# Optimization experiments

Measured on AMD Instinct MI355X. Metric: run time of the kernel, lower is better.

Reference implementation:

```python
import jax, jax.numpy as jnp
import numpy as np

WH, WW = 7, 7
N = WH * WW
DIM = 128
NH = 4
HD = DIM // NH
B_IMG, NW = 64, 64
B_ = B_IMG * NW

def _relative_position_index():
    ch = np.arange(WH)
    cw = np.arange(WW)
    coords = np.stack(np.meshgrid(ch, cw, indexing='ij'))  # (2, Wh, Ww)
    coords = coords.reshape(2, -1)  # (2, N)
    rel = coords[:, :, None] - coords[:, None, :]  # (2, N, N)
    rel = rel.transpose(1, 2, 0)  # (N, N, 2)
    rel[:, :, 0] += WH - 1
    rel[:, :, 1] += WW - 1
    rel[:, :, 0] *= 2 * WW - 1
    return jnp.asarray(rel.sum(-1), dtype=jnp.int32)  # (N, N)

REL_IDX = _relative_position_index()

def setup_inputs() -> dict:
    key = jax.random.key(0)
    k1, k2, k3, k4, k5 = jax.random.split(key, 5)
    return {
        'x': jax.random.normal(k1, (B_, N, DIM), dtype=jnp.float32),
        'mask': jax.random.normal(k2, (NW, N, N), dtype=jnp.float32),
        'qkv_w': jax.random.normal(k3, (3 * DIM, DIM), dtype=jnp.float32) * 0.02,
        'qkv_b': jax.random.normal(k4, (3 * DIM,), dtype=jnp.float32) * 0.02,
        'rel_table': jax.random.normal(k5, ((2 * WH - 1) * (2 * WW - 1), NH), dtype=jnp.float32) * 0.02,
    }

def reference(x, mask, qkv_w, qkv_b, rel_table):
    B_tot, n, c = x.shape
    scale = HD ** (-0.5)
    # qkv projection; torch split order is (nH, hD, qkv) innermost-to-outermost
    qkv = x @ qkv_w.T + qkv_b                      # (B_, N, 3C)
    qkv = qkv.reshape(B_tot, n, NH, HD, 3)
    q = jnp.transpose(qkv[..., 0], (0, 2, 1, 3))   # (B_, nH, N, hD)
    k = jnp.transpose(qkv[..., 1], (0, 2, 1, 3))
    v = jnp.transpose(qkv[..., 2], (0, 2, 1, 3))
    attn = jnp.einsum('bhnd,bhmd->bhnm', q, k) * scale  # (B_, nH, N, N)
    bias = jnp.transpose(rel_table[REL_IDX.reshape(-1)].reshape(n, n, NH), (2, 0, 1))
    attn = attn + bias[None]
    nW = mask.shape[0]
    attn = attn.reshape(B_tot // nW, nW, NH, n, n) + mask[None, :, None]
    attn = attn.reshape(B_tot, NH, n, n)
    attn = jax.nn.softmax(attn, axis=-1)
    out = jnp.einsum('bhnm,bhmd->bhnd', attn, v)   # (B_, nH, N, hD)
    return jnp.transpose(out, (0, 2, 1, 3)).reshape(B_tot, n, c)
```

## Files before the change

### kernel.cpp

```cpp
#include <hip/hip_runtime.h>


typedef short bf16x8 __attribute__((ext_vector_type(8)));
typedef float f32x4 __attribute__((ext_vector_type(4)));

#define DEVI __device__ __forceinline__

DEVI unsigned short f2b(float f) {
    unsigned u = __builtin_bit_cast(unsigned, f);
    u += 0x7fffu + ((u >> 16) & 1u);
    return (unsigned short)(u >> 16);
}

DEVI unsigned pack2(float lo, float hi) {
    return (unsigned)f2b(lo) | ((unsigned)f2b(hi) << 16);
}

#define WS_BIAS_OFF 98304
#define WS_COMB_OFF 131072
#define COMB_ELEMS  802816u
#define WS_NEED     (131072u + COMB_ELEMS * 4u)

__global__ __launch_bounds__(256) void prep_kernel(
    const float* __restrict__ qkvw, const float* __restrict__ qkvb,
    const float* __restrict__ maskg, const float* __restrict__ relt,
    unsigned short* __restrict__ wb, float* __restrict__ bb,
    float* __restrict__ comb)
{
    const int g = blockIdx.x * 256 + threadIdx.x;
    if (g < 49152) {
        const int row = g >> 7, col = g & 127;
        const int s = row >> 7, r7 = row & 127, hh = r7 >> 5, d = r7 & 31;
        const int c = hh * 96 + d * 3 + s;
        const float mul = (s == 0) ? 0.17677669529663687f : 1.0f;
        wb[row * 128 + col] = f2b(qkvw[c * 128 + col] * mul);
    } else if (g < 49536) {
        const int row = g - 49152;
        const int s = row >> 7, r7 = row & 127, hh = r7 >> 5, d = r7 & 31;
        const int c = hh * 96 + d * 3 + s;
        const float mul = (s == 0) ? 0.17677669529663687f : 1.0f;
        bb[row] = qkvb[c] * mul;
    } else {
        const unsigned g2 = (unsigned)(g - 49536);
        if (g2 < COMB_ELEMS) {
            const int wh = g2 / 3136;
            const int rr = g2 - wh * 3136;
            const int m = rr >> 6, n = rr & 63;
            const int w = wh >> 2, hh = wh & 3;
            float v = -1e30f;
            if (n < 49) {
                const int md = m / 7, mm = m - md * 7;
                const int nd = n / 7, nm = n - nd * 7;
                const int ridx = (md - nd + 6) * 13 + (mm - nm + 6);
                v = maskg[w * 2401 + m * 49 + n] + relt[ridx * 4 + hh];
            }
            comb[g2] = v;
        }
    }
}

struct __align__(16) SmemWS {
    unsigned short kk[4][64][32];
    union {
        unsigned short xs[64][136];
        unsigned short vt[4][32][72];
    } b;
};

__global__ __launch_bounds__(512, 6) void wattn_ws(
    const float* __restrict__ xg, const unsigned short* __restrict__ wb,
    const float* __restrict__ bb, const float* __restrict__ comb,
    float* __restrict__ outg)
{
    __shared__ SmemWS sm;
    const int tid  = threadIdx.x;
    const int lane = tid & 63;
    const int h    = (tid >> 6) & 3;
    const int half = tid >> 8;
    const int lr   = lane & 15;
    const int lq   = lane >> 4;
    const int bI   = blockIdx.x;

    const float* xb = xg + (size_t)bI * 6272;
    #pragma unroll
    for (int it = 0; it < 4; ++it) {
        int i = it * 512 + tid;
        if (i < 1568) {
            float4 v = ((const float4*)xb)[i];
            int row = i >> 5, col = (i & 31) << 2;
            *(ushort4*)&sm.b.xs[row][col] =
                make_ushort4(f2b(v.x), f2b(v.y), f2b(v.z), f2b(v.w));
        }
    }
    if (tid < 480) {
        int idx = tid << 2;
        *(ushort4*)&sm.b.xs[49 + (idx >> 7)][idx & 127] = make_ushort4(0, 0, 0, 0);
    }
    __syncthreads();

    bf16x8 af[4][2];
    #pragma unroll
    for (int ks = 0; ks < 4; ++ks)
        #pragma unroll
        for (int mtl = 0; mtl < 2; ++mtl)
            af[ks][mtl] = *(const bf16x8*)&sm.b.xs[(half * 2 + mtl) * 16 + lr][ks * 32 + lq * 8];
    __syncthreads();

    unsigned qfr[2][4];
    {
        f32x4 aq[2][2];
        __builtin_amdgcn_s_setprio(1);
        #pragma unroll
        for (int dh = 0; dh < 2; ++dh) {
            const int cp = h * 32 + dh * 16 + lr;
            aq[dh][0] = f32x4{0.f, 0.f, 0.f, 0.f};
            aq[dh][1] = f32x4{0.f, 0.f, 0.f, 0.f};
            #pragma unroll
            for (int ks = 0; ks < 4; ++ks) {
                bf16x8 wf = *(const bf16x8*)&wb[cp * 128 + ks * 32 + lq * 8];
                aq[dh][0] = __builtin_amdgcn_mfma_f32_16x16x32_bf16(wf, af[ks][0], aq[dh][0], 0, 0, 0);
                aq[dh][1] = __builtin_amdgcn_mfma_f32_16x16x32_bf16(wf, af[ks][1], aq[dh][1], 0, 0, 0);
            }
        }
        __builtin_amdgcn_s_setprio(0);
        unsigned pq[2][2][2];
        #pragma unroll
        for (int dh = 0; dh < 2; ++dh) {
            const float4 qb = *(const float4*)&bb[h * 32 + dh * 16 + lq * 4];
            #pragma unroll
            for (int mtl = 0; mtl < 2; ++mtl) {
                pq[dh][mtl][0] = pack2(aq[dh][mtl][0] + qb.x, aq[dh][mtl][1] + qb.y);
                pq[dh][mtl][1] = pack2(aq[dh][mtl][2] + qb.z, aq[dh][mtl][3] + qb.w);
            }
        }
        const int s0 = lr + ((lq & 1) * 2) * 16;
        const int s1 = s0 + 16;
        const bool hi = (lq >= 2);
        #pragma unroll
        for (int bl = 0; bl < 2; ++bl) {
            unsigned a0 = (unsigned)__shfl((int)pq[0][bl][0], s0);
            unsigned b0 = (unsigned)__shfl((int)pq[1][bl][0], s0);
            unsigned a1 = (unsigned)__shfl((int)pq[0][bl][1], s0);
            unsigned b1 = (unsigned)__shfl((int)pq[1][bl][1], s0);
            unsigned a2 = (unsigned)__shfl((int)pq[0][bl][0], s1);
            unsigned b2 = (unsigned)__shfl((int)pq[1][bl][0], s1);
            unsigned a3 = (unsigned)__shfl((int)pq[0][bl][1], s1);
            unsigned b3 = (unsigned)__shfl((int)pq[1][bl][1], s1);
            qfr[bl][0] = hi ? b0 : a0;
            qfr[bl][1] = hi ? b1 : a1;
            qfr[bl][2] = hi ? b2 : a2;
            qfr[bl][3] = hi ? b3 : a3;
        }
    }

    #pragma unroll
    for (int dh = 0; dh < 2; ++dh) {
        const int cp = 128 + h * 32 + dh * 16 + lr;
        const int dd = dh * 16 + lr;
        const float bc = bb[cp];
        f32x4 acc[2];
        acc[0] = f32x4{0.f, 0.f, 0.f, 0.f};
        acc[1] = f32x4{0.f, 0.f, 0.f, 0.f};
        __builtin_amdgcn_s_setprio(1);
        #pragma unroll
        for (int ks = 0; ks < 4; ++ks) {
            bf16x8 bf = *(const bf16x8*)&wb[cp * 128 + ks * 32 + lq * 8];
            #pragma unroll
            for (int mtl = 0; mtl < 2; ++mtl)
                acc[mtl] = __builtin_amdgcn_mfma_f32_16x16x32_bf16(af[ks][mtl], bf, acc[mtl], 0, 0, 0);
        }
        __builtin_amdgcn_s_setprio(0);
        #pragma unroll
        for (int mtl = 0; mtl < 2; ++mtl) {
            const int m0 = (half * 2 + mtl) * 16 + lq * 4;
            #pragma unroll
            for (int r = 0; r < 4; ++r)
                sm.kk[h][m0 + r][dd] = f2b(acc[mtl][r] + bc);
        }
    }

    #pragma unroll
    for (int dh = 0; dh < 2; ++dh) {
        const int cp = 256 + h * 32 + dh * 16 + lr;
        const int dd = dh * 16 + lr;
        const float bc = bb[cp];
        f32x4 acc[2];
        acc[0] = f32x4{0.f, 0.f, 0.f, 0.f};
        acc[1] = f32x4{0.f, 0.f, 0.f, 0.f};
        __builtin_amdgcn_s_setprio(1);
        #pragma unroll
        for (int ks = 0; ks < 4; ++ks) {
            bf16x8 bf = *(const bf16x8*)&wb[cp * 128 + ks * 32 + lq * 8];
            #pragma unroll
            for (int mtl = 0; mtl < 2; ++mtl)
                acc[mtl] = __builtin_amdgcn_mfma_f32_16x16x32_bf16(af[ks][mtl], bf, acc[mtl], 0, 0, 0);
        }
        __builtin_amdgcn_s_setprio(0);
        #pragma unroll
        for (int mtl = 0; mtl < 2; ++mtl) {
            const int m0 = (half * 2 + mtl) * 16 + lq * 4;
            *(ushort4*)&sm.b.vt[h][dd][m0] =
                make_ushort4(f2b(acc[mtl][0] + bc), f2b(acc[mtl][1] + bc),
                             f2b(acc[mtl][2] + bc), f2b(acc[mtl][3] + bc));
        }
    }
    __syncthreads();

    bf16x8 kf[4];
    #pragma unroll
    for (int t = 0; t < 4; ++t)
        kf[t] = *(const bf16x8*)&sm.kk[h][t * 16 + lr][lq * 8];

    const float* cwh = comb + (size_t)((bI & 63) * 4 + h) * 3136;
    float* ob = outg + (size_t)bI * 6272;
    const int src0 = ((lq & 1) * 2) * 16 + lr;
    const int src1 = src0 + 16;
    const bool up  = (lq >= 2);

    #pragma unroll
    for (int bl = 0; bl < 2; ++bl) {
        const int mt = half * 2 + bl;
        const int m  = mt * 16 + lr;
        const int mi = m < 48 ? m : 48;

        union { unsigned u[4]; bf16x8 v; } qu;
        qu.u[0] = qfr[bl][0]; qu.u[1] = qfr[bl][1];
        qu.u[2] = qfr[bl][2]; qu.u[3] = qfr[bl][3];

        const float* cr = cwh + mi * 64;
        f32x4 st[4];
        __builtin_amdgcn_s_setprio(1);
        #pragma unroll
        for (int a = 0; a < 4; ++a) {
            f32x4 cc = *(const f32x4*)&cr[a * 16 + lq * 4];
            st[a] = __builtin_amdgcn_mfma_f32_16x16x32_bf16(kf[a], qu.v, cc, 0, 0, 0);
        }
        __builtin_amdgcn_s_setprio(0);

        float mx = -3.4e38f;
        #pragma unroll
        for (int a = 0; a < 4; ++a)
            #pragma unroll
            for (int r = 0; r < 4; ++r) mx = fmaxf(mx, st[a][r]);
        mx = fmaxf(mx, __shfl_xor(mx, 16));
        mx = fmaxf(mx, __shfl_xor(mx, 32));
        float sum = 0.f;
        #pragma unroll
        for (int a = 0; a < 4; ++a)
            #pragma unroll
            for (int r = 0; r < 4; ++r) {
                float e = __expf(st[a][r] - mx);
                st[a][r] = e;
                sum += e;
            }
        sum += __shfl_xor(sum, 16);
        sum += __shfl_xor(sum, 32);
        const float inv = 1.f / sum;

        unsigned pk[4][2];
        #pragma unroll
        for (int a = 0; a < 4; ++a) {
            pk[a][0] = pack2(st[a][0] * inv, st[a][1] * inv);
            pk[a][1] = pack2(st[a][2] * inv, st[a][3] * inv);
        }

        f32x4 o[2];
        o[0] = f32x4{0.f, 0.f, 0.f, 0.f};
        o[1] = f32x4{0.f, 0.f, 0.f, 0.f};
        #pragma unroll
        for (int kt = 0; kt < 2; ++kt) {
            unsigned ea0 = (unsigned)__shfl((int)pk[2 * kt][0], src0);
            unsigned ea1 = (unsigned)__shfl((int)pk[2 * kt][1], src0);
            unsigned ea2 = (unsigned)__shfl((int)pk[2 * kt][0], src1);
            unsigned ea3 = (unsigned)__shfl((int)pk[2 * kt][1], src1);
            unsigned eb0 = (unsigned)__shfl((int)pk[2 * kt + 1][0], src0);
            unsigned eb1 = (unsigned)__shfl((int)pk[2 * kt + 1][1], src0);
            unsigned eb2 = (unsigned)__shfl((int)pk[2 * kt + 1][0], src1);
            unsigned eb3 = (unsigned)__shfl((int)pk[2 * kt + 1][1], src1);
            union { unsigned u[4]; bf16x8 v; } pu;
            pu.u[0] = up ? eb0 : ea0;
            pu.u[1] = up ? eb1 : ea1;
            pu.u[2] = up ? eb2 : ea2;
            pu.u[3] = up ? eb3 : ea3;
            __builtin_amdgcn_s_setprio(1);
            #pragma unroll
            for (int dt = 0; dt < 2; ++dt) {
                bf16x8 vf = *(const bf16x8*)&sm.b.vt[h][dt * 16 + lr][kt * 32 + lq * 8];
                o[dt] = __builtin_amdgcn_mfma_f32_16x16x32_bf16(vf, pu.v, o[dt], 0, 0, 0);
            }
            __builtin_amdgcn_s_setprio(0);
        }

        if (m < 49) {
            #pragma unroll
            for (int dt = 0; dt < 2; ++dt) {
                float4 v = make_float4(o[dt][0], o[dt][1], o[dt][2], o[dt][3]);
                *(float4*)&ob[m * 128 + h * 32 + dt * 16 + lq * 4] = v;
            }
        }
    }
}

struct __align__(16) SmemFB {
    unsigned short qk[2][4][64][32];
    union {
        unsigned short xs[64][136];
        unsigned short vt[4][32][72];
    } b;
};

__global__ __launch_bounds__(512, 6) void wattn_fb(
    const float* __restrict__ xg, const float* __restrict__ maskg,
    const float* __restrict__ qkvw, const float* __restrict__ qkvb,
    const float* __restrict__ relt, float* __restrict__ outg)
{
    __shared__ SmemFB sm;
    const int tid  = threadIdx.x;
    const int lane = tid & 63;
    const int wv   = tid >> 6;
    const int h    = wv & 3;
    const int half = wv >> 2;
    const int lr   = lane & 15;
    const int lq   = lane >> 4;
    const int bI   = blockIdx.x;

    const float* xb = xg + (size_t)bI * 6272;
    #pragma unroll
    for (int it = 0; it < 4; ++it) {
        int i = it * 512 + tid;
        if (i < 1568) {
            float4 v = ((const float4*)xb)[i];
            int row = i >> 5, col = (i & 31) << 2;
            *(ushort4*)&sm.b.xs[row][col] =
                make_ushort4(f2b(v.x), f2b(v.y), f2b(v.z), f2b(v.w));
        }
    }
    if (tid < 480) {
        int idx = tid << 2;
        *(ushort4*)&sm.b.xs[49 + (idx >> 7)][idx & 127] = make_ushort4(0, 0, 0, 0);
    }
    __syncthreads();

    bf16x8 af[4][2];
    #pragma unroll
    for (int ks = 0; ks < 4; ++ks)
        #pragma unroll
        for (int mtl = 0; mtl < 2; ++mtl)
            af[ks][mtl] = *(const bf16x8*)&sm.b.xs[(half * 2 + mtl) * 16 + lr][ks * 32 + lq * 8];
    __syncthreads();

    unsigned short* sbase = (unsigned short*)&sm;
    #pragma unroll
    for (int j = 0; j < 6; ++j) {
        const int c = (h * 6 + j) * 16 + lr;
        const float bc = qkvb[c];
        const int rem = j * 16 + lr;
        const int dd = rem / 3, s = rem % 3;
        const float mulv = (s == 0) ? 0.17677669529663687f : 1.0f;
        f32x4 acc[2];
        acc[0] = f32x4{0.f, 0.f, 0.f, 0.f};
        acc[1] = f32x4{0.f, 0.f, 0.f, 0.f};
        #pragma unroll
        for (int ks = 0; ks < 4; ++ks) {
            const float4* wp = (const float4*)(qkvw + c * 128 + ks * 32 + lq * 8);
            float4 w0 = wp[0], w1 = wp[1];
            bf16x8 t;
            t[0] = (short)f2b(w0.x); t[1] = (short)f2b(w0.y);
            t[2] = (short)f2b(w0.z); t[3] = (short)f2b(w0.w);
            t[4] = (short)f2b(w1.x); t[5] = (short)f2b(w1.y);
            t[6] = (short)f2b(w1.z); t[7] = (short)f2b(w1.w);
            #pragma unroll
            for (int mtl = 0; mtl < 2; ++mtl)
                acc[mtl] = __builtin_amdgcn_mfma_f32_16x16x32_bf16(af[ks][mtl], t, acc[mtl], 0, 0, 0);
        }
        #pragma unroll
        for (int mtl = 0; mtl < 2; ++mtl)
            #pragma unroll
            for (int r = 0; r < 4; ++r) {
                int m = (half * 2 + mtl) * 16 + lq * 4 + r;
                int soff = (s == 2) ? (16384 + (h * 32 + dd) * 72 + m)
                                    : (s * 8192 + h * 2048 + m * 32 + dd);
                sbase[soff] = f2b((acc[mtl][r] + bc) * mulv);
            }
    }
    __syncthreads();

    bf16x8 kf[4];
    #pragma unroll
    for (int t = 0; t < 4; ++t)
        kf[t] = *(const bf16x8*)&sm.qk[1][h][t * 16 + lr][lq * 8];

    const float* mw = maskg + (size_t)(bI & 63) * 2401;
    float* ob = outg + (size_t)bI * 6272;
    const int src0 = ((lq & 1) * 2) * 16 + lr;
    const int src1 = src0 + 16;
    const bool up  = (lq >= 2);

    #pragma unroll
    for (int bl = 0; bl < 2; ++bl) {
        const int mt = half * 2 + bl;
        const int m  = mt * 16 + lr;
        const int mi = m < 48 ? m : 48;

        f32x4 st[4];
        bf16x8 qf = *(const bf16x8*)&sm.qk[0][h][m][lq * 8];
        #pragma unroll
        for (int a = 0; a < 4; ++a) {
            f32x4 z = f32x4{0.f, 0.f, 0.f, 0.f};
            st[a] = __builtin_amdgcn_mfma_f32_16x16x32_bf16(kf[a], qf, z, 0, 0, 0);
        }
        const int md = mi / 7, mm = mi - md * 7;
        #pragma unroll
        for (int a = 0; a < 4; ++a)
            #pragma unroll
            for (int r = 0; r < 4; ++r) {
                int n = a * 16 + lq * 4 + r;
                int ni = n < 48 ? n : 48;
                int nd = ni / 7, nm = ni - nd * 7;
                int ridx = (md - nd + 6) * 13 + (mm - nm + 6);
                float v = st[a][r] + relt[ridx * 4 + h] + mw[mi * 49 + ni];
                st[a][r] = (n < 49) ? v : -1e30f;
            }

        float mx = -3.4e38f;
        #pragma unroll
        for (int a = 0; a < 4; ++a)
            #pragma unroll
            for (int r = 0; r < 4; ++r) mx = fmaxf(mx, st[a][r]);
        mx = fmaxf(mx, __shfl_xor(mx, 16));
        mx = fmaxf(mx, __shfl_xor(mx, 32));
        float sum = 0.f;
        #pragma unroll
        for (int a = 0; a < 4; ++a)
            #pragma unroll
            for (int r = 0; r < 4; ++r) {
                float e = __expf(st[a][r] - mx);
                st[a][r] = e;
                sum += e;
            }
        sum += __shfl_xor(sum, 16);
        sum += __shfl_xor(sum, 32);
        const float inv = 1.f / sum;

        unsigned pk[4][2];
        #pragma unroll
        for (int a = 0; a < 4; ++a) {
            pk[a][0] = pack2(st[a][0] * inv, st[a][1] * inv);
            pk[a][1] = pack2(st[a][2] * inv, st[a][3] * inv);
        }

        f32x4 o[2];
        o[0] = f32x4{0.f, 0.f, 0.f, 0.f};
        o[1] = f32x4{0.f, 0.f, 0.f, 0.f};
        #pragma unroll
        for (int kt = 0; kt < 2; ++kt) {
            unsigned ea0 = (unsigned)__shfl((int)pk[2 * kt][0], src0);
            unsigned ea1 = (unsigned)__shfl((int)pk[2 * kt][1], src0);
            unsigned ea2 = (unsigned)__shfl((int)pk[2 * kt][0], src1);
            unsigned ea3 = (unsigned)__shfl((int)pk[2 * kt][1], src1);
            unsigned eb0 = (unsigned)__shfl((int)pk[2 * kt + 1][0], src0);
            unsigned eb1 = (unsigned)__shfl((int)pk[2 * kt + 1][1], src0);
            unsigned eb2 = (unsigned)__shfl((int)pk[2 * kt + 1][0], src1);
            unsigned eb3 = (unsigned)__shfl((int)pk[2 * kt + 1][1], src1);
            union { unsigned u[4]; bf16x8 v; } pu;
            pu.u[0] = up ? eb0 : ea0;
            pu.u[1] = up ? eb1 : ea1;
            pu.u[2] = up ? eb2 : ea2;
            pu.u[3] = up ? eb3 : ea3;
            #pragma unroll
            for (int dt = 0; dt < 2; ++dt) {
                bf16x8 vf = *(const bf16x8*)&sm.b.vt[h][dt * 16 + lr][kt * 32 + lq * 8];
                o[dt] = __builtin_amdgcn_mfma_f32_16x16x32_bf16(vf, pu.v, o[dt], 0, 0, 0);
            }
        }

        if (m < 49) {
            #pragma unroll
            for (int dt = 0; dt < 2; ++dt) {
                float4 v = make_float4(o[dt][0], o[dt][1], o[dt][2], o[dt][3]);
                *(float4*)&ob[m * 128 + h * 32 + dt * 16 + lq * 4] = v;
            }
        }
    }
}

extern "C" void kernel_launch(void* const* d_in, const int* in_sizes, int n_in,
                              void* d_out, int out_size, void* d_ws, size_t ws_size,
                              hipStream_t stream) {
    const float* x    = (const float*)d_in[0];
    const float* mask = (const float*)d_in[1];
    const float* qkvw = (const float*)d_in[2];
    const float* qkvb = (const float*)d_in[3];
    const float* relt = (const float*)d_in[4];
    float* out = (float*)d_out;

    if (d_ws != nullptr && ws_size >= (size_t)WS_NEED) {
        unsigned short* wbf = (unsigned short*)d_ws;
        float* bbf  = (float*)((char*)d_ws + WS_BIAS_OFF);
        float* comb = (float*)((char*)d_ws + WS_COMB_OFF);
        prep_kernel<<<3330, 256, 0, stream>>>(qkvw, qkvb, mask, relt, wbf, bbf, comb);
        wattn_ws<<<4096, 512, 0, stream>>>(x, wbf, bbf, comb, out);
    } else {
        wattn_fb<<<4096, 512, 0, stream>>>(x, mask, qkvw, qkvb, relt, out);
    }
}
```

Before: 292.3 us.

## Make window-attention kernel persistent with register-prefetched next window input

The main kernel now launches a fixed grid of 768 blocks. Each block loops over windows with a stride equal to the grid size, and the input for the next window is loaded from global memory into registers while the current window is computed. The x staging buffer is no longer in a union with the V tile, so the prefetched tile can be written to shared memory without clobbering V, and the padding rows are zeroed only once. This is meant to hide global load latency and amortise launch and prologue cost, at the price of more shared memory and register pressure, which may lower occupancy. The s_setprio hints were also removed.

```diff
diff --git a/kernel.cpp b/kernel.cpp
--- a/kernel.cpp
+++ b/kernel.cpp
@@ -20,6 +20,7 @@
 #define WS_COMB_OFF 131072
 #define COMB_ELEMS  802816u
 #define WS_NEED     (131072u + COMB_ELEMS * 4u)
+#define GRID_WS     768
 
 __global__ __launch_bounds__(256) void prep_kernel(
     const float* __restrict__ qkvw, const float* __restrict__ qkvb,
@@ -61,11 +62,35 @@
 
 struct __align__(16) SmemWS {
     unsigned short kk[4][64][32];
-    union {
-        unsigned short xs[64][136];
-        unsigned short vt[4][32][72];
-    } b;
+    unsigned short vt[4][32][72];
+    unsigned short xs[64][136];
 };
+
+DEVI void stage_load(const float* __restrict__ xg, int w, int tid,
+                     float4& r0, float4& r1, float4& r2, float4& r3) {
+    const float4* xb = (const float4*)(xg + (size_t)w * 6272);
+    r0 = xb[tid];
+    r1 = xb[512 + tid];
+    r2 = xb[1024 + tid];
+    if (tid < 32) r3 = xb[1536 + tid];
+}
+
+DEVI void stage_write(unsigned short (*xs)[136], int tid,
+                      const float4& r0, const float4& r1,
+                      const float4& r2, const float4& r3) {
+    const int i0 = tid, i1 = 512 + tid, i2 = 1024 + tid;
+    *(ushort4*)&xs[i0 >> 5][(i0 & 31) << 2] =
+        make_ushort4(f2b(r0.x), f2b(r0.y), f2b(r0.z), f2b(r0.w));
+    *(ushort4*)&xs[i1 >> 5][(i1 & 31) << 2] =
+        make_ushort4(f2b(r1.x), f2b(r1.y), f2b(r1.z), f2b(r1.w));
+    *(ushort4*)&xs[i2 >> 5][(i2 & 31) << 2] =
+        make_ushort4(f2b(r2.x), f2b(r2.y), f2b(r2.z), f2b(r2.w));
+    if (tid < 32) {
+        const int i3 = 1536 + tid;
+        *(ushort4*)&xs[i3 >> 5][(i3 & 31) << 2] =
+            make_ushort4(f2b(r3.x), f2b(r3.y), f2b(r3.z), f2b(r3.w));
+    }
+}
 
 __global__ __launch_bounds__(512, 6) void wattn_ws(
     const float* __restrict__ xg, const unsigned short* __restrict__ wb,
@@ -79,6 +104,240 @@
     const int half = tid >> 8;
     const int lr   = lane & 15;
     const int lq   = lane >> 4;
+    const int bid  = blockIdx.x;
+
+    if (tid < 480) {
+        int idx = tid << 2;
+        *(ushort4*)&sm.xs[49 + (idx >> 7)][idx & 127] = make_ushort4(0, 0, 0, 0);
+    }
+
+    float4 rg0 = {0,0,0,0}, rg1 = {0,0,0,0}, rg2 = {0,0,0,0}, rg3 = {0,0,0,0};
+    stage_load(xg, bid, tid, rg0, rg1, rg2, rg3);
+    stage_write(sm.xs, tid, rg0, rg1, rg2, rg3);
+
+    const int s0x = lr + ((lq & 1) * 2) * 16;
+    const int s1x = s0x + 16;
+    const bool hi = (lq >= 2);
+
+    for (int w = bid; w < 4096; w += GRID_WS) {
+        __syncthreads();
+
+        bf16x8 af[4][2];
+        #pragma unroll
+        for (int ks = 0; ks < 4; ++ks)
+            #pragma unroll
+            for (int mtl = 0; mtl < 2; ++mtl)
+                af[ks][mtl] = *(const bf16x8*)&sm.xs[(half * 2 + mtl) * 16 + lr][ks * 32 + lq * 8];
+
+        const int wn = w + GRID_WS;
+        if (wn < 4096) stage_load(xg, wn, tid, rg0, rg1, rg2, rg3);
+
+        unsigned qfr[2][4];
+        {
+            f32x4 aq[2][2];
+            #pragma unroll
+            for (int dh = 0; dh < 2; ++dh) {
+                const int cp = h * 32 + dh * 16 + lr;
+                aq[dh][0] = f32x4{0.f, 0.f, 0.f, 0.f};
+                aq[dh][1] = f32x4{0.f, 0.f, 0.f, 0.f};
+                #pragma unroll
+                for (int ks = 0; ks < 4; ++ks) {
+                    bf16x8 wf = *(const bf16x8*)&wb[cp * 128 + ks * 32 + lq * 8];
+                    aq[dh][0] = __builtin_amdgcn_mfma_f32_16x16x32_bf16(wf, af[ks][0], aq[dh][0], 0, 0, 0);
+                    aq[dh][1] = __builtin_amdgcn_mfma_f32_16x16x32_bf16(wf, af[ks][1], aq[dh][1], 0, 0, 0);
+                }
+            }
+            unsigned pq[2][2][2];
+            #pragma unroll
+            for (int dh = 0; dh < 2; ++dh) {
+                const float4 qb = *(const float4*)&bb[h * 32 + dh * 16 + lq * 4];
+                #pragma unroll
+                for (int mtl = 0; mtl < 2; ++mtl) {
+                    pq[dh][mtl][0] = pack2(aq[dh][mtl][0] + qb.x, aq[dh][mtl][1] + qb.y);
+                    pq[dh][mtl][1] = pack2(aq[dh][mtl][2] + qb.z, aq[dh][mtl][3] + qb.w);
+                }
+            }
+            #pragma unroll
+            for (int bl = 0; bl < 2; ++bl) {
+                unsigned a0 = (unsigned)__shfl((int)pq[0][bl][0], s0x);
+                unsigned b0 = (unsigned)__shfl((int)pq[1][bl][0], s0x);
+                unsigned a1 = (unsigned)__shfl((int)pq[0][bl][1], s0x);
+                unsigned b1 = (unsigned)__shfl((int)pq[1][bl][1], s0x);
+                unsigned a2 = (unsigned)__shfl((int)pq[0][bl][0], s1x);
+                unsigned b2 = (unsigned)__shfl((int)pq[1][bl][0], s1x);
+                unsigned a3 = (unsigned)__shfl((int)pq[0][bl][1], s1x);
+                unsigned b3 = (unsigned)__shfl((int)pq[1][bl][1], s1x);
+                qfr[bl][0] = hi ? b0 : a0;
+                qfr[bl][1] = hi ? b1 : a1;
+                qfr[bl][2] = hi ? b2 : a2;
+                qfr[bl][3] = hi ? b3 : a3;
+            }
+        }
+
+        #pragma unroll
+        for (int dh = 0; dh < 2; ++dh) {
+            const int cp = 128 + h * 32 + dh * 16 + lr;
+            const int dd = dh * 16 + lr;
+            const float bc = bb[cp];
+            f32x4 acc[2];
+            acc[0] = f32x4{0.f, 0.f, 0.f, 0.f};
+            acc[1] = f32x4{0.f, 0.f, 0.f, 0.f};
+            #pragma unroll
+            for (int ks = 0; ks < 4; ++ks) {
+                bf16x8 bf = *(const bf16x8*)&wb[cp * 128 + ks * 32 + lq * 8];
+                #pragma unroll
+                for (int mtl = 0; mtl < 2; ++mtl)
+                    acc[mtl] = __builtin_amdgcn_mfma_f32_16x16x32_bf16(af[ks][mtl], bf, acc[mtl], 0, 0, 0);
+            }
+            #pragma unroll
+            for (int mtl = 0; mtl < 2; ++mtl) {
+                const int m0 = (half * 2 + mtl) * 16 + lq * 4;
+                #pragma unroll
+                for (int r = 0; r < 4; ++r)
+                    sm.kk[h][m0 + r][dd] = f2b(acc[mtl][r] + bc);
+            }
+        }
+
+        #pragma unroll
+        for (int dh = 0; dh < 2; ++dh) {
+            const int cp = 256 + h * 32 + dh * 16 + lr;
+            const int dd = dh * 16 + lr;
+            const float bc = bb[cp];
+            f32x4 acc[2];
+            acc[0] = f32x4{0.f, 0.f, 0.f, 0.f};
+            acc[1] = f32x4{0.f, 0.f, 0.f, 0.f};
+            #pragma unroll
+            for (int ks = 0; ks < 4; ++ks) {
+                bf16x8 bf = *(const bf16x8*)&wb[cp * 128 + ks * 32 + lq * 8];
+                #pragma unroll
+                for (int mtl = 0; mtl < 2; ++mtl)
+                    acc[mtl] = __builtin_amdgcn_mfma_f32_16x16x32_bf16(af[ks][mtl], bf, acc[mtl], 0, 0, 0);
+            }
+            #pragma unroll
+            for (int mtl = 0; mtl < 2; ++mtl) {
+                const int m0 = (half * 2 + mtl) * 16 + lq * 4;
+                *(ushort4*)&sm.vt[h][dd][m0] =
+                    make_ushort4(f2b(acc[mtl][0] + bc), f2b(acc[mtl][1] + bc),
+                                 f2b(acc[mtl][2] + bc), f2b(acc[mtl][3] + bc));
+            }
+        }
+        __syncthreads();
+
+        bf16x8 kf[4];
+        #pragma unroll
+        for (int t = 0; t < 4; ++t)
+            kf[t] = *(const bf16x8*)&sm.kk[h][t * 16 + lr][lq * 8];
+
+        const float* cwh = comb + (size_t)((w & 63) * 4 + h) * 3136;
+        float* ob = outg + (size_t)w * 6272;
+        const int src0 = ((lq & 1) * 2) * 16 + lr;
+        const int src1 = src0 + 16;
+        const bool up  = (lq >= 2);
+
+        #pragma unroll
+        for (int bl = 0; bl < 2; ++bl) {
+            const int mt = half * 2 + bl;
+            const int m  = mt * 16 + lr;
+            const int mi = m < 48 ? m : 48;
+
+            union { unsigned u[4]; bf16x8 v; } qu;
+            qu.u[0] = qfr[bl][0]; qu.u[1] = qfr[bl][1];
+            qu.u[2] = qfr[bl][2]; qu.u[3] = qfr[bl][3];
+
+            const float* cr = cwh + mi * 64;
+            f32x4 st[4];
+            #pragma unroll
+            for (int a = 0; a < 4; ++a) {
+                f32x4 cc = *(const f32x4*)&cr[a * 16 + lq * 4];
+                st[a] = __builtin_amdgcn_mfma_f32_16x16x32_bf16(kf[a], qu.v, cc, 0, 0, 0);
+            }
+
+            float mx = -3.4e38f;
+            #pragma unroll
+            for (int a = 0; a < 4; ++a)
+                #pragma unroll
+                for (int r = 0; r < 4; ++r) mx = fmaxf(mx, st[a][r]);
+            mx = fmaxf(mx, __shfl_xor(mx, 16));
+            mx = fmaxf(mx, __shfl_xor(mx, 32));
+            float sum = 0.f;
+            #pragma unroll
+            for (int a = 0; a < 4; ++a)
+                #pragma unroll
+                for (int r = 0; r < 4; ++r) {
+                    float e = __expf(st[a][r] - mx);
+                    st[a][r] = e;
+                    sum += e;
+                }
+            sum += __shfl_xor(sum, 16);
+            sum += __shfl_xor(sum, 32);
+            const float inv = 1.f / sum;
+
+            unsigned pk[4][2];
+            #pragma unroll
+            for (int a = 0; a < 4; ++a) {
+                pk[a][0] = pack2(st[a][0] * inv, st[a][1] * inv);
+                pk[a][1] = pack2(st[a][2] * inv, st[a][3] * inv);
+            }
+
+            f32x4 o[2];
+            o[0] = f32x4{0.f, 0.f, 0.f, 0.f};
+            o[1] = f32x4{0.f, 0.f, 0.f, 0.f};
+            #pragma unroll
+            for (int kt = 0; kt < 2; ++kt) {
+                unsigned ea0 = (unsigned)__shfl((int)pk[2 * kt][0], src0);
+                unsigned ea1 = (unsigned)__shfl((int)pk[2 * kt][1], src0);
+                unsigned ea2 = (unsigned)__shfl((int)pk[2 * kt][0], src1);
+                unsigned ea3 = (unsigned)__shfl((int)pk[2 * kt][1], src1);
+                unsigned eb0 = (unsigned)__shfl((int)pk[2 * kt + 1][0], src0);
+                unsigned eb1 = (unsigned)__shfl((int)pk[2 * kt + 1][1], src0);
+                unsigned eb2 = (unsigned)__shfl((int)pk[2 * kt + 1][0], src1);
+                unsigned eb3 = (unsigned)__shfl((int)pk[2 * kt + 1][1], src1);
+                union { unsigned u[4]; bf16x8 v; } pu;
+                pu.u[0] = up ? eb0 : ea0;
+                pu.u[1] = up ? eb1 : ea1;
+                pu.u[2] = up ? eb2 : ea2;
+                pu.u[3] = up ? eb3 : ea3;
+                #pragma unroll
+                for (int dt = 0; dt < 2; ++dt) {
+                    bf16x8 vf = *(const bf16x8*)&sm.vt[h][dt * 16 + lr][kt * 32 + lq * 8];
+                    o[dt] = __builtin_amdgcn_mfma_f32_16x16x32_bf16(vf, pu.v, o[dt], 0, 0, 0);
+                }
+            }
+
+            if (m < 49) {
+                #pragma unroll
+                for (int dt = 0; dt < 2; ++dt) {
+                    float4 v = make_float4(o[dt][0], o[dt][1], o[dt][2], o[dt][3]);
+                    *(float4*)&ob[m * 128 + h * 32 + dt * 16 + lq * 4] = v;
+                }
+            }
+        }
+
+        if (wn < 4096) stage_write(sm.xs, tid, rg0, rg1, rg2, rg3);
+    }
+}
+
+struct __align__(16) SmemFB {
+    unsigned short qk[2][4][64][32];
+    union {
+        unsigned short xs[64][136];
+        unsigned short vt[4][32][72];
+    } b;
+};
+
+__global__ __launch_bounds__(512, 6) void wattn_fb(
+    const float* __restrict__ xg, const float* __restrict__ maskg,
+    const float* __restrict__ qkvw, const float* __restrict__ qkvb,
+    const float* __restrict__ relt, float* __restrict__ outg)
+{
+    __shared__ SmemFB sm;
+    const int tid  = threadIdx.x;
+    const int lane = tid & 63;
+    const int wv   = tid >> 6;
+    const int h    = wv & 3;
+    const int half = wv >> 2;
+    const int lr   = lane & 15;
+    const int lq   = lane >> 4;
     const int bI   = blockIdx.x;
 
     const float* xb = xg + (size_t)bI * 6272;
@@ -106,112 +365,48 @@
             af[ks][mtl] = *(const bf16x8*)&sm.b.xs[(half * 2 + mtl) * 16 + lr][ks * 32 + lq * 8];
     __syncthreads();
 
-    unsigned qfr[2][4];
-    {
-        f32x4 aq[2][2];
-        __builtin_amdgcn_s_setprio(1);
-        #pragma unroll
-        for (int dh = 0; dh < 2; ++dh) {
-            const int cp = h * 32 + dh * 16 + lr;
-            aq[dh][0] = f32x4{0.f, 0.f, 0.f, 0.f};
-            aq[dh][1] = f32x4{0.f, 0.f, 0.f, 0.f};
-            #pragma unroll
-            for (int ks = 0; ks < 4; ++ks) {
-                bf16x8 wf = *(const bf16x8*)&wb[cp * 128 + ks * 32 + lq * 8];
-                aq[dh][0] = __builtin_amdgcn_mfma_f32_16x16x32_bf16(wf, af[ks][0], aq[dh][0], 0, 0, 0);
-                aq[dh][1] = __builtin_amdgcn_mfma_f32_16x16x32_bf16(wf, af[ks][1], aq[dh][1], 0, 0, 0);
-            }
-        }
-        __builtin_amdgcn_s_setprio(0);
-        unsigned pq[2][2][2];
-        #pragma unroll
-        for (int dh = 0; dh < 2; ++dh) {
-            const float4 qb = *(const float4*)&bb[h * 32 + dh * 16 + lq * 4];
-            #pragma unroll
-            for (int mtl = 0; mtl < 2; ++mtl) {
-                pq[dh][mtl][0] = pack2(aq[dh][mtl][0] + qb.x, aq[dh][mtl][1] + qb.y);
-                pq[dh][mtl][1] = pack2(aq[dh][mtl][2] + qb.z, aq[dh][mtl][3] + qb.w);
-            }
-        }
-        const int s0 = lr + ((lq & 1) * 2) * 16;
-        const int s1 = s0 + 16;
-        const bool hi = (lq >= 2);
-        #pragma unroll
-        for (int bl = 0; bl < 2; ++bl) {
-            unsigned a0 = (unsigned)__shfl((int)pq[0][bl][0], s0);
-            unsigned b0 = (unsigned)__shfl((int)pq[1][bl][0], s0);
-            unsigned a1 = (unsigned)__shfl((int)pq[0][bl][1], s0);
-            unsigned b1 = (unsigned)__shfl((int)pq[1][bl][1], s0);
-            unsigned a2 = (unsigned)__shfl((int)pq[0][bl][0], s1);
-            unsigned b2 = (unsigned)__shfl((int)pq[1][bl][0], s1);
-            unsigned a3 = (unsigned)__shfl((int)pq[0][bl][1], s1);
-            unsigned b3 = (unsigned)__shfl((int)pq[1][bl][1], s1);
-            qfr[bl][0] = hi ? b0 : a0;
-            qfr[bl][1] = hi ? b1 : a1;
-            qfr[bl][2] = hi ? b2 : a2;
-            qfr[bl][3] = hi ? b3 : a3;
-        }
-    }
-
+    unsigned short* sbase = (unsigned short*)&sm;
     #pragma unroll
-    for (int dh = 0; dh < 2; ++dh) {
-        const int cp = 128 + h * 32 + dh * 16 + lr;
-        const int dd = dh * 16 + lr;
-        const float bc = bb[cp];
+    for (int j = 0; j < 6; ++j) {
+        const int c = (h * 6 + j) * 16 + lr;
+        const float bc = qkvb[c];
+        const int rem = j * 16 + lr;
+        const int dd = rem / 3, s = rem % 3;
+        const float mulv = (s == 0) ? 0.17677669529663687f : 1.0f;
         f32x4 acc[2];
         acc[0] = f32x4{0.f, 0.f, 0.f, 0.f};
         acc[1] = f32x4{0.f, 0.f, 0.f, 0.f};
-        __builtin_amdgcn_s_setprio(1);
         #pragma unroll
         for (int ks = 0; ks < 4; ++ks) {
-            bf16x8 bf = *(const bf16x8*)&wb[cp * 128 + ks * 32 + lq * 8];
+            const float4* wp = (const float4*)(qkvw + c * 128 + ks * 32 + lq * 8);
+            float4 w0 = wp[0], w1 = wp[1];
+            bf16x8 t;
+            t[0] = (short)f2b(w0.x); t[1] = (short)f2b(w0.y);
+            t[2] = (short)f2b(w0.z); t[3] = (short)f2b(w0.w);
+            t[4] = (short)f2b(w1.x); t[5] = (short)f2b(w1.y);
+            t[6] = (short)f2b(w1.z); t[7] = (short)f2b(w1.w);
             #pragma unroll
             for (int mtl = 0; mtl < 2; ++mtl)
-                acc[mtl] = __builtin_amdgcn_mfma_f32_16x16x32_bf16(af[ks][mtl], bf, acc[mtl], 0, 0, 0);
-        }
-        __builtin_amdgcn_s_setprio(0);
-        #pragma unroll
-        for (int mtl = 0; mtl < 2; ++mtl) {
-            const int m0 = (half * 2 + mtl) * 16 + lq * 4;
-            #pragma unroll
-            for (int r = 0; r < 4; ++r)
-                sm.kk[h][m0 + r][dd] = f2b(acc[mtl][r] + bc);
-        }
-    }
-
-    #pragma unroll
-    for (int dh = 0; dh < 2; ++dh) {
-        const int cp = 256 + h * 32 + dh * 16 + lr;
-        const int dd = dh * 16 + lr;
-        const float bc = bb[cp];
-        f32x4 acc[2];
-        acc[0] = f32x4{0.f, 0.f, 0.f, 0.f};
-        acc[1] = f32x4{0.f, 0.f, 0.f, 0.f};
-        __builtin_amdgcn_s_setprio(1);
-        #pragma unroll
-        for (int ks = 0; ks < 4; ++ks) {
-            bf16x8 bf = *(const bf16x8*)&wb[cp * 128 + ks * 32 + lq * 8];
-            #pragma unroll
-            for (int mtl = 0; mtl < 2; ++mtl)
-                acc[mtl] = __builtin_amdgcn_mfma_f32_16x16x32_bf16(af[ks][mtl], bf, acc[mtl], 0, 0, 0);
-        }
-        __builtin_amdgcn_s_setprio(0);
-        #pragma unroll
-        for (int mtl = 0; mtl < 2; ++mtl) {
-            const int m0 = (half * 2 + mtl) * 16 + lq * 4;
-            *(ushort4*)&sm.b.vt[h][dd][m0] =
-                make_ushort4(f2b(acc[mtl][0] + bc), f2b(acc[mtl][1] + bc),
-                             f2b(acc[mtl][2] + bc), f2b(acc[mtl][3] + bc));
-        }
+                acc[mtl] = __builtin_amdgcn_mfma_f32_16x16x32_bf16(af[ks][mtl], t, acc[mtl], 0, 0, 0);
+        }
+        #pragma unroll
+        for (int mtl = 0; mtl < 2; ++mtl)
+            #pragma unroll
+            for (int r = 0; r < 4; ++r) {
+                int m = (half * 2 + mtl) * 16 + lq * 4 + r;
+                int soff = (s == 2) ? (16384 + (h * 32 + dd) * 72 + m)
+                                    : (s * 8192 + h * 2048 + m * 32 + dd);
+                sbase[soff] = f2b((acc[mtl][r] + bc) * mulv);
+            }
     }
     __syncthreads();
 
     bf16x8 kf[4];
     #pragma unroll
     for (int t = 0; t < 4; ++t)
-        kf[t] = *(const bf16x8*)&sm.kk[h][t * 16 + lr][lq * 8];
-
-    const float* cwh = comb + (size_t)((bI & 63) * 4 + h) * 3136;
+        kf[t] = *(const bf16x8*)&sm.qk[1][h][t * 16 + lr][lq * 8];
+
+    const float* mw = maskg + (size_t)(bI & 63) * 2401;
     float* ob = outg + (size_t)bI * 6272;
     const int src0 = ((lq & 1) * 2) * 16 + lr;
     const int src1 = src0 + 16;
@@ -223,19 +418,25 @@
         const int m  = mt * 16 + lr;
         const int mi = m < 48 ? m : 48;
 
-        union { unsigned u[4]; bf16x8 v; } qu;
-        qu.u[0] = qfr[bl][0]; qu.u[1] = qfr[bl][1];
-        qu.u[2] = qfr[bl][2]; qu.u[3] = qfr[bl][3];
-
-        const float* cr = cwh + mi * 64;
         f32x4 st[4];
-        __builtin_amdgcn_s_setprio(1);
+        bf16x8 qf = *(const bf16x8*)&sm.qk[0][h][m][lq * 8];
         #pragma unroll
         for (int a = 0; a < 4; ++a) {
-            f32x4 cc = *(const f32x4*)&cr[a * 16 + lq * 4];
-            st[a] = __builtin_amdgcn_mfma_f32_16x16x32_bf16(kf[a], qu.v, cc, 0, 0, 0);
-        }
-        __builtin_amdgcn_s_setprio(0);
+            f32x4 z = f32x4{0.f, 0.f, 0.f, 0.f};
+            st[a] = __builtin_amdgcn_mfma_f32_16x16x32_bf16(kf[a], qf, z, 0, 0, 0);
+        }
+        const int md = mi / 7, mm = mi - md * 7;
+        #pragma unroll
+        for (int a = 0; a < 4; ++a)
+            #pragma unroll
+            for (int r = 0; r < 4; ++r) {
+                int n = a * 16 + lq * 4 + r;
+                int ni = n < 48 ? n : 48;
+                int nd = ni / 7, nm = ni - nd * 7;
+                int ridx = (md - nd + 6) * 13 + (mm - nm + 6);
+                float v = st[a][r] + relt[ridx * 4 + h] + mw[mi * 49 + ni];
+                st[a][r] = (n < 49) ? v : -1e30f;
+            }
 
         float mx = -3.4e38f;
         #pragma unroll
@@ -282,191 +483,6 @@
             pu.u[1] = up ? eb1 : ea1;
             pu.u[2] = up ? eb2 : ea2;
             pu.u[3] = up ? eb3 : ea3;
-            __builtin_amdgcn_s_setprio(1);
-            #pragma unroll
-            for (int dt = 0; dt < 2; ++dt) {
-                bf16x8 vf = *(const bf16x8*)&sm.b.vt[h][dt * 16 + lr][kt * 32 + lq * 8];
-                o[dt] = __builtin_amdgcn_mfma_f32_16x16x32_bf16(vf, pu.v, o[dt], 0, 0, 0);
-            }
-            __builtin_amdgcn_s_setprio(0);
-        }
-
-        if (m < 49) {
-            #pragma unroll
-            for (int dt = 0; dt < 2; ++dt) {
-                float4 v = make_float4(o[dt][0], o[dt][1], o[dt][2], o[dt][3]);
-                *(float4*)&ob[m * 128 + h * 32 + dt * 16 + lq * 4] = v;
-            }
-        }
-    }
-}
-
-struct __align__(16) SmemFB {
-    unsigned short qk[2][4][64][32];
-    union {
-        unsigned short xs[64][136];
-        unsigned short vt[4][32][72];
-    } b;
-};
-
-__global__ __launch_bounds__(512, 6) void wattn_fb(
-    const float* __restrict__ xg, const float* __restrict__ maskg,
-    const float* __restrict__ qkvw, const float* __restrict__ qkvb,
-    const float* __restrict__ relt, float* __restrict__ outg)
-{
-    __shared__ SmemFB sm;
-    const int tid  = threadIdx.x;
-    const int lane = tid & 63;
-    const int wv   = tid >> 6;
-    const int h    = wv & 3;
-    const int half = wv >> 2;
-    const int lr   = lane & 15;
-    const int lq   = lane >> 4;
-    const int bI   = blockIdx.x;
-
-    const float* xb = xg + (size_t)bI * 6272;
-    #pragma unroll
-    for (int it = 0; it < 4; ++it) {
-        int i = it * 512 + tid;
-        if (i < 1568) {
-            float4 v = ((const float4*)xb)[i];
-            int row = i >> 5, col = (i & 31) << 2;
-            *(ushort4*)&sm.b.xs[row][col] =
-                make_ushort4(f2b(v.x), f2b(v.y), f2b(v.z), f2b(v.w));
-        }
-    }
-    if (tid < 480) {
-        int idx = tid << 2;
-        *(ushort4*)&sm.b.xs[49 + (idx >> 7)][idx & 127] = make_ushort4(0, 0, 0, 0);
-    }
-    __syncthreads();
-
-    bf16x8 af[4][2];
-    #pragma unroll
-    for (int ks = 0; ks < 4; ++ks)
-        #pragma unroll
-        for (int mtl = 0; mtl < 2; ++mtl)
-            af[ks][mtl] = *(const bf16x8*)&sm.b.xs[(half * 2 + mtl) * 16 + lr][ks * 32 + lq * 8];
-    __syncthreads();
-
-    unsigned short* sbase = (unsigned short*)&sm;
-    #pragma unroll
-    for (int j = 0; j < 6; ++j) {
-        const int c = (h * 6 + j) * 16 + lr;
-        const float bc = qkvb[c];
-        const int rem = j * 16 + lr;
-        const int dd = rem / 3, s = rem % 3;
-        const float mulv = (s == 0) ? 0.17677669529663687f : 1.0f;
-        f32x4 acc[2];
-        acc[0] = f32x4{0.f, 0.f, 0.f, 0.f};
-        acc[1] = f32x4{0.f, 0.f, 0.f, 0.f};
-        #pragma unroll
-        for (int ks = 0; ks < 4; ++ks) {
-            const float4* wp = (const float4*)(qkvw + c * 128 + ks * 32 + lq * 8);
-            float4 w0 = wp[0], w1 = wp[1];
-            bf16x8 t;
-            t[0] = (short)f2b(w0.x); t[1] = (short)f2b(w0.y);
-            t[2] = (short)f2b(w0.z); t[3] = (short)f2b(w0.w);
-            t[4] = (short)f2b(w1.x); t[5] = (short)f2b(w1.y);
-            t[6] = (short)f2b(w1.z); t[7] = (short)f2b(w1.w);
-            #pragma unroll
-            for (int mtl = 0; mtl < 2; ++mtl)
-                acc[mtl] = __builtin_amdgcn_mfma_f32_16x16x32_bf16(af[ks][mtl], t, acc[mtl], 0, 0, 0);
-        }
-        #pragma unroll
-        for (int mtl = 0; mtl < 2; ++mtl)
-            #pragma unroll
-            for (int r = 0; r < 4; ++r) {
-                int m = (half * 2 + mtl) * 16 + lq * 4 + r;
-                int soff = (s == 2) ? (16384 + (h * 32 + dd) * 72 + m)
-                                    : (s * 8192 + h * 2048 + m * 32 + dd);
-                sbase[soff] = f2b((acc[mtl][r] + bc) * mulv);
-            }
-    }
-    __syncthreads();
-
-    bf16x8 kf[4];
-    #pragma unroll
-    for (int t = 0; t < 4; ++t)
-        kf[t] = *(const bf16x8*)&sm.qk[1][h][t * 16 + lr][lq * 8];
-
-    const float* mw = maskg + (size_t)(bI & 63) * 2401;
-    float* ob = outg + (size_t)bI * 6272;
-    const int src0 = ((lq & 1) * 2) * 16 + lr;
-    const int src1 = src0 + 16;
-    const bool up  = (lq >= 2);
-
-    #pragma unroll
-    for (int bl = 0; bl < 2; ++bl) {
-        const int mt = half * 2 + bl;
-        const int m  = mt * 16 + lr;
-        const int mi = m < 48 ? m : 48;
-
-        f32x4 st[4];
-        bf16x8 qf = *(const bf16x8*)&sm.qk[0][h][m][lq * 8];
-        #pragma unroll
-        for (int a = 0; a < 4; ++a) {
-            f32x4 z = f32x4{0.f, 0.f, 0.f, 0.f};
-            st[a] = __builtin_amdgcn_mfma_f32_16x16x32_bf16(kf[a], qf, z, 0, 0, 0);
-        }
-        const int md = mi / 7, mm = mi - md * 7;
-        #pragma unroll
-        for (int a = 0; a < 4; ++a)
-            #pragma unroll
-            for (int r = 0; r < 4; ++r) {
-                int n = a * 16 + lq * 4 + r;
-                int ni = n < 48 ? n : 48;
-                int nd = ni / 7, nm = ni - nd * 7;
-                int ridx = (md - nd + 6) * 13 + (mm - nm + 6);
-                float v = st[a][r] + relt[ridx * 4 + h] + mw[mi * 49 + ni];
-                st[a][r] = (n < 49) ? v : -1e30f;
-            }
-
-        float mx = -3.4e38f;
-        #pragma unroll
-        for (int a = 0; a < 4; ++a)
-            #pragma unroll
-            for (int r = 0; r < 4; ++r) mx = fmaxf(mx, st[a][r]);
-        mx = fmaxf(mx, __shfl_xor(mx, 16));
-        mx = fmaxf(mx, __shfl_xor(mx, 32));
-        float sum = 0.f;
-        #pragma unroll
-        for (int a = 0; a < 4; ++a)
-            #pragma unroll
-            for (int r = 0; r < 4; ++r) {
-                float e = __expf(st[a][r] - mx);
-                st[a][r] = e;
-                sum += e;
-            }
-        sum += __shfl_xor(sum, 16);
-        sum += __shfl_xor(sum, 32);
-        const float inv = 1.f / sum;
-
-        unsigned pk[4][2];
-        #pragma unroll
-        for (int a = 0; a < 4; ++a) {
-            pk[a][0] = pack2(st[a][0] * inv, st[a][1] * inv);
-            pk[a][1] = pack2(st[a][2] * inv, st[a][3] * inv);
-        }
-
-        f32x4 o[2];
-        o[0] = f32x4{0.f, 0.f, 0.f, 0.f};
-        o[1] = f32x4{0.f, 0.f, 0.f, 0.f};
-        #pragma unroll
-        for (int kt = 0; kt < 2; ++kt) {
-            unsigned ea0 = (unsigned)__shfl((int)pk[2 * kt][0], src0);
-            unsigned ea1 = (unsigned)__shfl((int)pk[2 * kt][1], src0);
-            unsigned ea2 = (unsigned)__shfl((int)pk[2 * kt][0], src1);
-            unsigned ea3 = (unsigned)__shfl((int)pk[2 * kt][1], src1);
-            unsigned eb0 = (unsigned)__shfl((int)pk[2 * kt + 1][0], src0);
-            unsigned eb1 = (unsigned)__shfl((int)pk[2 * kt + 1][1], src0);
-            unsigned eb2 = (unsigned)__shfl((int)pk[2 * kt + 1][0], src1);
-            unsigned eb3 = (unsigned)__shfl((int)pk[2 * kt + 1][1], src1);
-            union { unsigned u[4]; bf16x8 v; } pu;
-            pu.u[0] = up ? eb0 : ea0;
-            pu.u[1] = up ? eb1 : ea1;
-            pu.u[2] = up ? eb2 : ea2;
-            pu.u[3] = up ? eb3 : ea3;
             #pragma unroll
             for (int dt = 0; dt < 2; ++dt) {
                 bf16x8 vf = *(const bf16x8*)&sm.b.vt[h][dt * 16 + lr][kt * 32 + lq * 8];
@@ -499,7 +515,7 @@
         float* bbf  = (float*)((char*)d_ws + WS_BIAS_OFF);
         float* comb = (float*)((char*)d_ws + WS_COMB_OFF);
         prep_kernel<<<3330, 256, 0, stream>>>(qkvw, qkvb, mask, relt, wbf, bbf, comb);
-        wattn_ws<<<4096, 512, 0, stream>>>(x, wbf, bbf, comb, out);
+        wattn_ws<<<GRID_WS, 512, 0, stream>>>(x, wbf, bbf, comb, out);
     } else {
         wattn_fb<<<4096, 512, 0, stream>>>(x, mask, qkvw, qkvb, relt, out);
     }
```

New measurement: 486.5 us. +66.4%, slower.
